# Kernel optimization log

Measured on AMD Instinct MI355X. Metric: run time of the kernel, lower is better.

## Reference

```python
import jax, jax.numpy as jnp
import numpy as np
from functools import partial

HID = 256
HOR = 5

def _lin(k, i, o):
    return jax.random.normal(k, (i, o), jnp.float32) / np.sqrt(i)

def setup_inputs() -> dict:
    key = jax.random.key(0)
    ks = jax.random.split(key, 32)
    B, T, D, Hf, Wf = 4, 16, 768, 16, 16
    H, W = 1024, 1024
    inp = {}
    inp['features'] = jax.random.normal(ks[0], (B, T, D, Hf, Wf), jnp.float32)
    inp['predictions'] = jax.random.uniform(ks[1], (B, T, 1, H, W), dtype=jnp.float32)
    # position encoder: 4 -> HID -> HID
    inp['pe_w1'] = _lin(ks[2], 4, HID); inp['pe_b1'] = jnp.zeros((HID,), jnp.float32)
    inp['pe_w2'] = _lin(ks[3], HID, HID); inp['pe_b2'] = jnp.zeros((HID,), jnp.float32)
    # 2-layer LSTM, gate order i,f,g,o (torch convention)
    inp['wih0'] = _lin(ks[4], HID, 4 * HID); inp['whh0'] = _lin(ks[5], HID, 4 * HID)
    inp['bih0'] = jnp.zeros((4 * HID,), jnp.float32); inp['bhh0'] = jnp.zeros((4 * HID,), jnp.float32)
    inp['wih1'] = _lin(ks[6], HID, 4 * HID); inp['whh1'] = _lin(ks[7], HID, 4 * HID)
    inp['bih1'] = jnp.zeros((4 * HID,), jnp.float32); inp['bhh1'] = jnp.zeros((4 * HID,), jnp.float32)
    # motion predictor: HID -> HID -> HID/2 -> HOR*4
    inp['mp_w1'] = _lin(ks[8], HID, HID); inp['mp_b1'] = jnp.zeros((HID,), jnp.float32)
    inp['mp_w2'] = _lin(ks[9], HID, HID // 2); inp['mp_b2'] = jnp.zeros((HID // 2,), jnp.float32)
    inp['mp_w3'] = _lin(ks[10], HID // 2, HOR * 4); inp['mp_b3'] = jnp.zeros((HOR * 4,), jnp.float32)
    # confidence: HID -> HID/2 -> HOR
    inp['cf_w1'] = _lin(ks[11], HID, HID // 2); inp['cf_b1'] = jnp.zeros((HID // 2,), jnp.float32)
    inp['cf_w2'] = _lin(ks[12], HID // 2, HOR); inp['cf_b2'] = jnp.zeros((HOR,), jnp.float32)
    return inp

def _extract_bboxes(predictions):
    # predictions: (B,T,1,H,W) -> bboxes (B,T,4) in (cx,cy,w,h), normalized
    B, T, _, H, W = predictions.shape
    mask = predictions[:, :, 0] > 0.5  # (B,T,H,W)
    xs = jnp.arange(W, dtype=jnp.float32)           # (W,)
    ys = jnp.arange(H, dtype=jnp.float32)[:, None]  # (H,1)
    big = jnp.float32(H + W)
    x_min = jnp.min(jnp.where(mask, xs, big), axis=(-2, -1))
    x_max = jnp.max(jnp.where(mask, xs, -1.0), axis=(-2, -1))
    y_min = jnp.min(jnp.where(mask, ys, big), axis=(-2, -1))
    y_max = jnp.max(jnp.where(mask, ys, -1.0), axis=(-2, -1))
    has = jnp.any(mask, axis=(-2, -1))  # (B,T)
    cx = (x_min + x_max) / 2.0 / W
    cy = (y_min + y_max) / 2.0 / H
    w = (x_max - x_min) / W
    h = (y_max - y_min) / H
    bbox = jnp.stack([cx, cy, w, h], axis=-1)  # (B,T,4)
    default = jnp.array([0.5, 0.5, 0.1, 0.1], dtype=jnp.float32)
    return jnp.where(has[..., None], bbox, default)

def _lstm_layer(x, wih, whh, bih, bhh):
    # x: (B,T,HID); returns (hs (B,T,H), h_final (B,H))
    B = x.shape[0]
    xg = jnp.einsum('bti,ig->btg', x, wih) + bih  # (B,T,4H)
    def step(carry, xg_t):
        h, c = carry
        g = xg_t + h @ whh + bhh
        i, f, gg, o = jnp.split(g, 4, axis=-1)
        i = jax.nn.sigmoid(i); f = jax.nn.sigmoid(f)
        gg = jnp.tanh(gg); o = jax.nn.sigmoid(o)
        c = f * c + i * gg
        h = o * jnp.tanh(c)
        return (h, c), h
    z = jnp.zeros((B, HID), x.dtype)
    (h, c), hs = jax.lax.scan(step, (z, z), xg.swapaxes(0, 1))
    return hs.swapaxes(0, 1), h

def reference(features, predictions, pe_w1, pe_b1, pe_w2, pe_b2,
              wih0, whh0, bih0, bhh0, wih1, whh1, bih1, bhh1,
              mp_w1, mp_b1, mp_w2, mp_b2, mp_w3, mp_b3,
              cf_w1, cf_b1, cf_w2, cf_b2):
    B, T = features.shape[:2]
    bboxes = _extract_bboxes(predictions)  # (B,T,4)
    pos = jax.nn.relu(bboxes @ pe_w1 + pe_b1)
    pos = jax.nn.relu(pos @ pe_w2 + pe_b2)  # (B,T,HID)
    h1, _ = _lstm_layer(pos, wih0, whh0, bih0, bhh0)
    motion_features, last_hidden = _lstm_layer(h1, wih1, whh1, bih1, bhh1)
    x = jax.nn.relu(last_hidden @ mp_w1 + mp_b1)
    x = jax.nn.relu(x @ mp_w2 + mp_b2)
    predicted_deltas = (x @ mp_w3 + mp_b3).reshape(B, HOR, 4)
    last_bbox = bboxes[:, -1:, :]
    predicted_bboxes = last_bbox + jnp.cumsum(predicted_deltas, axis=1)
    c = jax.nn.relu(last_hidden @ cf_w1 + cf_b1)
    confidence = jax.nn.sigmoid(c @ cf_w2 + cf_b2)  # (B,HOR)
    predicted_locations = predicted_bboxes[..., :2]
    predicted_scales = predicted_bboxes[..., 2:]
    return (predicted_deltas, predicted_bboxes, predicted_locations,
            predicted_scales, motion_features, confidence, bboxes)
```

## Files before the change

### kernel.cpp

```cpp
#include <hip/hip_runtime.h>
#include <math.h>

#define BIGI (1 << 30)

#define PM_OFF    0
#define HT0_OFF   8192
#define HT2_OFF   40960
#define DONE_OFF  45056
#define ZERO_BEG  8192
#define ZERO_END  45057

#define OUT_DELTAS 0
#define OUT_PBB    80
#define OUT_LOC    160
#define OUT_SCL    200
#define OUT_MF     240
#define OUT_CONF   16624
#define OUT_BBOX   16644

__device__ __forceinline__ float sigmoidf_(float x) { return 1.0f / (1.0f + expf(-x)); }

__device__ __forceinline__ void storeh(unsigned long long* p, float h, int tag) {
    unsigned long long v =
        ((unsigned long long)(unsigned)tag << 32) | (unsigned long long)__float_as_uint(h);
    __hip_atomic_store(p, v, __ATOMIC_RELAXED, __HIP_MEMORY_SCOPE_AGENT);
}
__device__ __forceinline__ float pollh(const unsigned long long* p, int tag) {
    unsigned long long v = __hip_atomic_load(p, __ATOMIC_RELAXED, __HIP_MEMORY_SCOPE_AGENT);
    while ((int)(v >> 32) != tag) {
        __builtin_amdgcn_s_sleep(1);
        v = __hip_atomic_load(p, __ATOMIC_RELAXED, __HIP_MEMORY_SCOPE_AGENT);
    }
    return __uint_as_float((unsigned)v);
}
__device__ __forceinline__ float2 pollh2(const unsigned long long* p1, int tag1,
                                         const unsigned long long* p2, int tag2) {
    unsigned long long v1 = __hip_atomic_load(p1, __ATOMIC_RELAXED, __HIP_MEMORY_SCOPE_AGENT);
    unsigned long long v2 = __hip_atomic_load(p2, __ATOMIC_RELAXED, __HIP_MEMORY_SCOPE_AGENT);
    while ((int)(v1 >> 32) != tag1) {
        __builtin_amdgcn_s_sleep(1);
        v1 = __hip_atomic_load(p1, __ATOMIC_RELAXED, __HIP_MEMORY_SCOPE_AGENT);
    }
    while ((int)(v2 >> 32) != tag2) {
        __builtin_amdgcn_s_sleep(1);
        v2 = __hip_atomic_load(p2, __ATOMIC_RELAXED, __HIP_MEMORY_SCOPE_AGENT);
    }
    return make_float2(__uint_as_float((unsigned)v1), __uint_as_float((unsigned)v2));
}

__global__ __launch_bounds__(256) void k_minmax(const float4* __restrict__ pred,
                                                int* __restrict__ ws) {
    int tid = threadIdx.x;
    for (int i = ZERO_BEG + blockIdx.x * 256 + tid; i < ZERO_END; i += 2048 * 256)
        ws[i] = 0;
    int img = blockIdx.x >> 5;
    int chunk = blockIdx.x & 31;
    int base = img * 262144 + chunk * 8192 + tid;
    int xmn = BIGI, xmx = -1, ymn = BIGI, ymx = -1;
#pragma unroll 4
    for (int i = 0; i < 32; ++i) {
        int idx4 = base + i * 256;
        float4 v = pred[idx4];
        int x = (idx4 << 2) & 1023;
        int y = (idx4 >> 8) & 1023;
        bool m0 = v.x > 0.5f, m1 = v.y > 0.5f, m2 = v.z > 0.5f, m3 = v.w > 0.5f;
        int cmn = m0 ? x : (m1 ? x + 1 : (m2 ? x + 2 : (m3 ? x + 3 : BIGI)));
        int cmx = m3 ? x + 3 : (m2 ? x + 2 : (m1 ? x + 1 : (m0 ? x : -1)));
        xmn = min(xmn, cmn);
        xmx = max(xmx, cmx);
        if (m0 | m1 | m2 | m3) { ymn = min(ymn, y); ymx = max(ymx, y); }
    }
    for (int off = 32; off > 0; off >>= 1) {
        xmn = min(xmn, __shfl_down(xmn, off));
        xmx = max(xmx, __shfl_down(xmx, off));
        ymn = min(ymn, __shfl_down(ymn, off));
        ymx = max(ymx, __shfl_down(ymx, off));
    }
    __shared__ int red[4][4];
    int wave = tid >> 6;
    if ((tid & 63) == 0) { red[0][wave] = xmn; red[1][wave] = xmx; red[2][wave] = ymn; red[3][wave] = ymx; }
    __syncthreads();
    if (tid == 0) {
        xmn = min(min(red[0][0], red[0][1]), min(red[0][2], red[0][3]));
        xmx = max(max(red[1][0], red[1][1]), max(red[1][2], red[1][3]));
        ymn = min(min(red[2][0], red[2][1]), min(red[2][2], red[2][3]));
        ymx = max(max(red[3][0], red[3][1]), max(red[3][2], red[3][3]));
        ((int4*)(ws + PM_OFF))[blockIdx.x] = make_int4(xmn, xmx, ymn, ymx);
    }
}

__device__ __forceinline__ void mk_bbox(int xmn, int xmx, int ymn, int ymx, float* o) {
    if (xmx >= 0) {
        o[0] = (float)(xmn + xmx) * (0.5f / 1024.0f);
        o[1] = (float)(ymn + ymx) * (0.5f / 1024.0f);
        o[2] = (float)(xmx - xmn) * (1.0f / 1024.0f);
        o[3] = (float)(ymx - ymn) * (1.0f / 1024.0f);
    } else { o[0] = 0.5f; o[1] = 0.5f; o[2] = 0.1f; o[3] = 0.1f; }
}

__global__ __launch_bounds__(256, 1) void k_fused(
    const float* __restrict__ pe_w1, const float* __restrict__ pe_b1,
    const float* __restrict__ pe_w2, const float* __restrict__ pe_b2,
    const float* __restrict__ wih0, const float* __restrict__ whh0,
    const float* __restrict__ bih0, const float* __restrict__ bhh0,
    const float* __restrict__ wih1, const float* __restrict__ whh1,
    const float* __restrict__ bih1, const float* __restrict__ bhh1,
    const float* __restrict__ mp_w1, const float* __restrict__ mp_b1,
    const float* __restrict__ mp_w2, const float* __restrict__ mp_b2,
    const float* __restrict__ mp_w3, const float* __restrict__ mp_b3,
    const float* __restrict__ cf_w1, const float* __restrict__ cf_b1,
    const float* __restrict__ cf_w2, const float* __restrict__ cf_b2,
    const int4* __restrict__ pm4, unsigned long long* __restrict__ hT0,
    unsigned long long* __restrict__ hT2, int* __restrict__ done,
    float* __restrict__ out) {
    __shared__ __align__(16) float sPX[4096];
    __shared__ __align__(16) float sP1[4096];
    __shared__ float xgl[1024];
    __shared__ __align__(16) float hsm[256];
    __shared__ __align__(16) float h2sm[256];
    __shared__ float partA[256];
    __shared__ float sBB[64];
    const int tid = threadIdx.x, blk = blockIdx.x;

    if (blk >= 128) {
        float a0 = 0.f, a1 = 1.f, a2 = 2.f, a3 = 3.f, a4 = 4.f, a5 = 5.f, a6 = 6.f, a7 = 7.f;
        const float m = 1.0000001f, c = 0.9999999f;
        for (;;) {
#pragma unroll 8
            for (int i = 0; i < 512; ++i) {
                a0 = fmaf(a0, m, c); a1 = fmaf(a1, m, c); a2 = fmaf(a2, m, c); a3 = fmaf(a3, m, c);
                a4 = fmaf(a4, m, c); a5 = fmaf(a5, m, c); a6 = fmaf(a6, m, c); a7 = fmaf(a7, m, c);
            }
            if (__hip_atomic_load(done, __ATOMIC_RELAXED, __HIP_MEMORY_SCOPE_AGENT) >= 4) break;
        }
        asm volatile("" :: "v"(a0), "v"(a1), "v"(a2), "v"(a3), "v"(a4), "v"(a5), "v"(a6), "v"(a7));
        return;
    }

    const int layer = blk >> 6;
    const int b = (blk >> 4) & 3, g = blk & 15;
    const int cidx = tid & 63, kq = tid >> 6;
    const int gate = cidx >> 4, u = cidx & 15;
    const int col = gate * 256 + g * 16 + u;
    const int krow0 = kq * 64;

    const float* wih = layer ? wih1 : wih0;
    const float* whh = layer ? whh1 : whh0;
    const float* bih = layer ? bih1 : bih0;
    const float* bhh = layer ? bhh1 : bhh0;

    float4 wvi[16];
#pragma unroll
    for (int k4 = 0; k4 < 16; ++k4) {
        int r = krow0 + k4 * 4;
        wvi[k4].x = wih[(r + 0) * 1024 + col];
        wvi[k4].y = wih[(r + 1) * 1024 + col];
        wvi[k4].z = wih[(r + 2) * 1024 + col];
        wvi[k4].w = wih[(r + 3) * 1024 + col];
    }

    if (layer == 0) {
        {
            int il = tid >> 4, c2 = (tid & 15) * 2;
            int4 A = pm4[(b * 16 + il) * 32 + c2];
            int4 B = pm4[(b * 16 + il) * 32 + c2 + 1];
            int xmn = min(A.x, B.x), xmx = max(A.y, B.y);
            int ymn = min(A.z, B.z), ymx = max(A.w, B.w);
            for (int off = 8; off > 0; off >>= 1) {
                xmn = min(xmn, __shfl_down(xmn, off, 16));
                xmx = max(xmx, __shfl_down(xmx, off, 16));
                ymn = min(ymn, __shfl_down(ymn, off, 16));
                ymx = max(ymx, __shfl_down(ymx, off, 16));
            }
            if ((tid & 15) == 0) {
                float bb[4];
                mk_bbox(xmn, xmx, ymn, ymx, bb);
                sBB[il * 4 + 0] = bb[0]; sBB[il * 4 + 1] = bb[1];
                sBB[il * 4 + 2] = bb[2]; sBB[il * 4 + 3] = bb[3];
                if (g == 0) {
                    out[OUT_BBOX + (b * 16 + il) * 4 + 0] = bb[0];
                    out[OUT_BBOX + (b * 16 + il) * 4 + 1] = bb[1];
                    out[OUT_BBOX + (b * 16 + il) * 4 + 2] = bb[2];
                    out[OUT_BBOX + (b * 16 + il) * 4 + 3] = bb[3];
                }
            }
        }
        __syncthreads();
        {
            float w0 = pe_w1[tid], w1 = pe_w1[256 + tid];
            float w2 = pe_w1[512 + tid], w3 = pe_w1[768 + tid], b1v = pe_b1[tid];
#pragma unroll
            for (int i = 0; i < 16; ++i) {
                float v = sBB[i * 4] * w0 + sBB[i * 4 + 1] * w1 +
                          sBB[i * 4 + 2] * w2 + sBB[i * 4 + 3] * w3 + b1v;
                sP1[i * 256 + tid] = fmaxf(v, 0.0f);
            }
        }
        __syncthreads();
        {
            float acc[16];
            float b2v = pe_b2[tid];
#pragma unroll
            for (int i = 0; i < 16; ++i) acc[i] = b2v;
            for (int k = 0; k < 256; ++k) {
                float wv = pe_w2[k * 256 + tid];
#pragma unroll
                for (int i = 0; i < 16; ++i) acc[i] += sP1[i * 256 + k] * wv;
            }
#pragma unroll
            for (int i = 0; i < 16; ++i) sPX[i * 256 + tid] = fmaxf(acc[i], 0.0f);
        }
        __syncthreads();
        float bsum = 0.0f;
        if (tid < 64) {
            int cc = (tid >> 4) * 256 + g * 16 + (tid & 15);
            bsum = bih[cc] + bhh[cc];
        }
        for (int t = 0; t < 16; ++t) {
            const float4* xr = (const float4*)&sPX[t * 256 + krow0];
            float a = 0.0f;
#pragma unroll
            for (int k = 0; k < 16; ++k) {
                float4 x = xr[k];
                a += x.x * wvi[k].x + x.y * wvi[k].y + x.z * wvi[k].z + x.w * wvi[k].w;
            }
            partA[tid] = a;
            __syncthreads();
            if (tid < 64)
                xgl[t * 64 + tid] = partA[tid] + partA[64 + tid] +
                                    partA[128 + tid] + partA[192 + tid] + bsum;
            __syncthreads();
        }
    }

    float4 wvh[16];
#pragma unroll
    for (int k4 = 0; k4 < 16; ++k4) {
        int r = krow0 + k4 * 4;
        wvh[k4].x = whh[(r + 0) * 1024 + col];
        wvh[k4].y = whh[(r + 1) * 1024 + col];
        wvh[k4].z = whh[(r + 2) * 1024 + col];
        wvh[k4].w = whh[(r + 3) * 1024 + col];
    }
    float bs0 = 0.f, bs1 = 0.f, bs2 = 0.f, bs3 = 0.f;
    if (layer == 1 && tid < 16) {
        int uu = g * 16 + tid;
        bs0 = bih[uu] + bhh[uu];
        bs1 = bih[256 + uu] + bhh[256 + uu];
        bs2 = bih[512 + uu] + bhh[512 + uu];
        bs3 = bih[768 + uu] + bhh[768 + uu];
    }

    float cst = 0.0f;
    for (int t = 0; t < 16; ++t) {
        if (layer == 0) {
            if (t) hsm[tid] = pollh(&hT0[((b * 16 + t - 1) << 8) + tid], t);
        } else {
            if (t) {
                float2 hv = pollh2(&hT0[((b * 16 + t) << 8) + tid], t + 1,
                                   &hT2[(((b << 1) | ((t - 1) & 1)) << 8) + tid], t);
                hsm[tid] = hv.x; h2sm[tid] = hv.y;
            } else {
                hsm[tid] = pollh(&hT0[((b * 16) << 8) + tid], 1);
            }
        }
        __syncthreads();
        float a = 0.0f;
        if (layer == 0) {
            if (t) {
                const float4* hr = (const float4*)&hsm[krow0];
#pragma unroll
                for (int k = 0; k < 16; ++k) {
                    float4 h = hr[k];
                    a += h.x * wvh[k].x + h.y * wvh[k].y + h.z * wvh[k].z + h.w * wvh[k].w;
                }
            }
        } else {
            const float4* xr = (const float4*)&hsm[krow0];
#pragma unroll
            for (int k = 0; k < 16; ++k) {
                float4 x = xr[k];
                a += x.x * wvi[k].x + x.y * wvi[k].y + x.z * wvi[k].z + x.w * wvi[k].w;
            }
            if (t) {
                const float4* hr = (const float4*)&h2sm[krow0];
#pragma unroll
                for (int k = 0; k < 16; ++k) {
                    float4 h = hr[k];
                    a += h.x * wvh[k].x + h.y * wvh[k].y + h.z * wvh[k].z + h.w * wvh[k].w;
                }
            }
        }
        partA[tid] = a;
        __syncthreads();
        if (tid < 16) {
            float gi, gf, gg, go;
            if (layer == 0) {
                gi = xgl[t * 64 + tid];       gf = xgl[t * 64 + 16 + tid];
                gg = xgl[t * 64 + 32 + tid];  go = xgl[t * 64 + 48 + tid];
            } else { gi = bs0; gf = bs1; gg = bs2; go = bs3; }
#pragma unroll
            for (int q = 0; q < 4; ++q) {
                gi += partA[q * 64 + tid];
                gf += partA[q * 64 + 16 + tid];
                gg += partA[q * 64 + 32 + tid];
                go += partA[q * 64 + 48 + tid];
            }
            float i_ = sigmoidf_(gi), f_ = sigmoidf_(gf);
            float g_ = tanhf(gg), o_ = sigmoidf_(go);
            cst = f_ * cst + i_ * g_;
            float h = o_ * tanhf(cst);
            int unit = g * 16 + tid;
            if (layer == 0) {
                storeh(&hT0[((b * 16 + t) << 8) + unit], h, t + 1);
            } else {
                storeh(&hT2[(((b << 1) | (t & 1)) << 8) + unit], h, t + 1);
                out[OUT_MF + (b * 16 + t) * 256 + unit] = h;
            }
        }
    }
    if (layer == 0 || g != 0) return;

    float* lh = sPX;
    float* x1 = sPX + 256;
    float* c1 = sPX + 512;
    float* x2 = sPX + 640;
    float* dl = sPX + 768;
    lh[tid] = pollh(&hT2[(((b << 1) | 1) << 8) + tid], 16);
    if (tid < 32) {
        int4 v = pm4[(b * 16 + 15) * 32 + tid];
        int xmn = v.x, xmx = v.y, ymn = v.z, ymx = v.w;
        for (int off = 16; off > 0; off >>= 1) {
            xmn = min(xmn, __shfl_down(xmn, off, 32));
            xmx = max(xmx, __shfl_down(xmx, off, 32));
            ymn = min(ymn, __shfl_down(ymn, off, 32));
            ymx = max(ymx, __shfl_down(ymx, off, 32));
        }
        if (tid == 0) mk_bbox(xmn, xmx, ymn, ymx, sBB);
    }
    __syncthreads();
    {
        float a = mp_b1[tid];
#pragma unroll 4
        for (int k = 0; k < 256; ++k) a += lh[k] * mp_w1[k * 256 + tid];
        x1[tid] = fmaxf(a, 0.0f);
    }
    if (tid < 128) {
        float a = cf_b1[tid];
#pragma unroll 4
        for (int k = 0; k < 256; ++k) a += lh[k] * cf_w1[k * 128 + tid];
        c1[tid] = fmaxf(a, 0.0f);
    }
    __syncthreads();
    if (tid < 128) {
        float a = mp_b2[tid];
#pragma unroll 4
        for (int k = 0; k < 256; ++k) a += x1[k] * mp_w2[k * 128 + tid];
        x2[tid] = fmaxf(a, 0.0f);
    } else if (tid < 133) {
        int jj = tid - 128;
        float a = cf_b2[jj];
#pragma unroll 4
        for (int k = 0; k < 128; ++k) a += c1[k] * cf_w2[k * 5 + jj];
        out[OUT_CONF + b * 5 + jj] = sigmoidf_(a);
    }
    __syncthreads();
    if (tid < 20) {
        float a = mp_b3[tid];
#pragma unroll 4
        for (int k = 0; k < 128; ++k) a += x2[k] * mp_w3[k * 20 + tid];
        dl[tid] = a;
        out[OUT_DELTAS + b * 20 + tid] = a;
    }
    __syncthreads();
    if (tid < 4) {
        float acc = sBB[tid];
        for (int hh = 0; hh < 5; ++hh) {
            acc += dl[hh * 4 + tid];
            out[OUT_PBB + b * 20 + hh * 4 + tid] = acc;
            if (tid < 2) out[OUT_LOC + b * 10 + hh * 2 + tid] = acc;
            else out[OUT_SCL + b * 10 + hh * 2 + (tid - 2)] = acc;
        }
    }
    __syncthreads();
    if (tid == 0) atomicAdd(done, 1);
}

extern "C" void kernel_launch(void* const* d_in, const int* in_sizes, int n_in,
                              void* d_out, int out_size, void* d_ws, size_t ws_size,
                              hipStream_t stream) {
    (void)in_sizes; (void)n_in; (void)out_size; (void)ws_size;
    const float* pred = (const float*)d_in[1];
    const float* pe_w1 = (const float*)d_in[2];
    const float* pe_b1 = (const float*)d_in[3];
    const float* pe_w2 = (const float*)d_in[4];
    const float* pe_b2 = (const float*)d_in[5];
    const float* wih0 = (const float*)d_in[6];
    const float* whh0 = (const float*)d_in[7];
    const float* bih0 = (const float*)d_in[8];
    const float* bhh0 = (const float*)d_in[9];
    const float* wih1 = (const float*)d_in[10];
    const float* whh1 = (const float*)d_in[11];
    const float* bih1 = (const float*)d_in[12];
    const float* bhh1 = (const float*)d_in[13];
    const float* mp_w1 = (const float*)d_in[14];
    const float* mp_b1 = (const float*)d_in[15];
    const float* mp_w2 = (const float*)d_in[16];
    const float* mp_b2 = (const float*)d_in[17];
    const float* mp_w3 = (const float*)d_in[18];
    const float* mp_b3 = (const float*)d_in[19];
    const float* cf_w1 = (const float*)d_in[20];
    const float* cf_b1 = (const float*)d_in[21];
    const float* cf_w2 = (const float*)d_in[22];
    const float* cf_b2 = (const float*)d_in[23];
    float* out = (float*)d_out;
    int* wsi = (int*)d_ws;

    hipLaunchKernelGGL(k_minmax, dim3(64 * 32), dim3(256), 0, stream,
                       (const float4*)pred, wsi);
    hipLaunchKernelGGL(k_fused, dim3(256), dim3(256), 0, stream,
                       pe_w1, pe_b1, pe_w2, pe_b2,
                       wih0, whh0, bih0, bhh0,
                       wih1, whh1, bih1, bhh1,
                       mp_w1, mp_b1, mp_w2, mp_b2, mp_w3, mp_b3,
                       cf_w1, cf_b1, cf_w2, cf_b2,
                       (const int4*)(wsi + PM_OFF),
                       (unsigned long long*)(wsi + HT0_OFF),
                       (unsigned long long*)(wsi + HT2_OFF),
                       wsi + DONE_OFF, out);
}
```

Baseline: 594.4 us.

## Drop spinner blocks and batch layer-0 input projection before recurrence

Removes the 128 busy-spin 'heater' blocks and the done counter, so the fused kernel launches only the 128 LSTM worker blocks. Layer-0 now computes the input projection for all 16 timesteps as one batched pass into shared memory, then loads the recurrent weights only afterwards, so the two weight sets are never held in registers together. The confidence head's first layer moves onto otherwise idle threads. The spinners were presumably meant to keep clocks high or hold CUs, so removing them risks lower clocks or slower inter-block polling latency.

```diff
diff --git a/kernel.cpp b/kernel.cpp
--- a/kernel.cpp
+++ b/kernel.cpp
@@ -6,9 +6,8 @@
 #define PM_OFF    0
 #define HT0_OFF   8192
 #define HT2_OFF   40960
-#define DONE_OFF  45056
 #define ZERO_BEG  8192
-#define ZERO_END  45057
+#define ZERO_END  45056
 
 #define OUT_DELTAS 0
 #define OUT_PBB    80
@@ -51,8 +50,10 @@
 __global__ __launch_bounds__(256) void k_minmax(const float4* __restrict__ pred,
                                                 int* __restrict__ ws) {
     int tid = threadIdx.x;
-    for (int i = ZERO_BEG + blockIdx.x * 256 + tid; i < ZERO_END; i += 2048 * 256)
-        ws[i] = 0;
+    {
+        int i = ZERO_BEG + blockIdx.x * 256 + tid;
+        if (i < ZERO_END) ws[i] = 0;
+    }
     int img = blockIdx.x >> 5;
     int chunk = blockIdx.x & 31;
     int base = img * 262144 + chunk * 8192 + tid;
@@ -111,55 +112,24 @@
     const float* __restrict__ cf_w1, const float* __restrict__ cf_b1,
     const float* __restrict__ cf_w2, const float* __restrict__ cf_b2,
     const int4* __restrict__ pm4, unsigned long long* __restrict__ hT0,
-    unsigned long long* __restrict__ hT2, int* __restrict__ done,
-    float* __restrict__ out) {
-    __shared__ __align__(16) float sPX[4096];
-    __shared__ __align__(16) float sP1[4096];
+    unsigned long long* __restrict__ hT2, float* __restrict__ out) {
+    __shared__ __align__(16) float sA[4096];
+    __shared__ __align__(16) float sB[4096];
     __shared__ float xgl[1024];
     __shared__ __align__(16) float hsm[256];
     __shared__ __align__(16) float h2sm[256];
-    __shared__ float partA[256];
+    __shared__ float part[256];
     __shared__ float sBB[64];
     const int tid = threadIdx.x, blk = blockIdx.x;
-
-    if (blk >= 128) {
-        float a0 = 0.f, a1 = 1.f, a2 = 2.f, a3 = 3.f, a4 = 4.f, a5 = 5.f, a6 = 6.f, a7 = 7.f;
-        const float m = 1.0000001f, c = 0.9999999f;
-        for (;;) {
-#pragma unroll 8
-            for (int i = 0; i < 512; ++i) {
-                a0 = fmaf(a0, m, c); a1 = fmaf(a1, m, c); a2 = fmaf(a2, m, c); a3 = fmaf(a3, m, c);
-                a4 = fmaf(a4, m, c); a5 = fmaf(a5, m, c); a6 = fmaf(a6, m, c); a7 = fmaf(a7, m, c);
-            }
-            if (__hip_atomic_load(done, __ATOMIC_RELAXED, __HIP_MEMORY_SCOPE_AGENT) >= 4) break;
-        }
-        asm volatile("" :: "v"(a0), "v"(a1), "v"(a2), "v"(a3), "v"(a4), "v"(a5), "v"(a6), "v"(a7));
-        return;
-    }
-
-    const int layer = blk >> 6;
+    const int stage = blk >> 6;
     const int b = (blk >> 4) & 3, g = blk & 15;
-    const int cidx = tid & 63, kq = tid >> 6;
-    const int gate = cidx >> 4, u = cidx & 15;
-    const int col = gate * 256 + g * 16 + u;
+    const int cq = tid & 63, kq = tid >> 6;
+    const int col = ((cq >> 4) << 8) + g * 16 + (cq & 15);
     const int krow0 = kq * 64;
 
-    const float* wih = layer ? wih1 : wih0;
-    const float* whh = layer ? whh1 : whh0;
-    const float* bih = layer ? bih1 : bih0;
-    const float* bhh = layer ? bhh1 : bhh0;
-
-    float4 wvi[16];
-#pragma unroll
-    for (int k4 = 0; k4 < 16; ++k4) {
-        int r = krow0 + k4 * 4;
-        wvi[k4].x = wih[(r + 0) * 1024 + col];
-        wvi[k4].y = wih[(r + 1) * 1024 + col];
-        wvi[k4].z = wih[(r + 2) * 1024 + col];
-        wvi[k4].w = wih[(r + 3) * 1024 + col];
-    }
-
-    if (layer == 0) {
+    float cst = 0.0f;
+
+    if (stage == 0) {
         {
             int il = tid >> 4, c2 = (tid & 15) * 2;
             int4 A = pm4[(b * 16 + il) * 32 + c2];
@@ -193,7 +163,7 @@
             for (int i = 0; i < 16; ++i) {
                 float v = sBB[i * 4] * w0 + sBB[i * 4 + 1] * w1 +
                           sBB[i * 4 + 2] * w2 + sBB[i * 4 + 3] * w3 + b1v;
-                sP1[i * 256 + tid] = fmaxf(v, 0.0f);
+                sB[i * 256 + tid] = fmaxf(v, 0.0f);
             }
         }
         __syncthreads();
@@ -205,127 +175,159 @@
             for (int k = 0; k < 256; ++k) {
                 float wv = pe_w2[k * 256 + tid];
 #pragma unroll
-                for (int i = 0; i < 16; ++i) acc[i] += sP1[i * 256 + k] * wv;
-            }
-#pragma unroll
-            for (int i = 0; i < 16; ++i) sPX[i * 256 + tid] = fmaxf(acc[i], 0.0f);
-        }
-        __syncthreads();
-        float bsum = 0.0f;
-        if (tid < 64) {
-            int cc = (tid >> 4) * 256 + g * 16 + (tid & 15);
-            bsum = bih[cc] + bhh[cc];
-        }
+                for (int i = 0; i < 16; ++i) acc[i] += sB[i * 256 + k] * wv;
+            }
+#pragma unroll
+            for (int i = 0; i < 16; ++i) sA[i * 256 + tid] = fmaxf(acc[i], 0.0f);
+        }
+        __syncthreads();
+        {
+            float4 wt[16];
+#pragma unroll
+            for (int k4 = 0; k4 < 16; ++k4) {
+                int r = krow0 + k4 * 4;
+                wt[k4].x = wih0[(r + 0) * 1024 + col];
+                wt[k4].y = wih0[(r + 1) * 1024 + col];
+                wt[k4].z = wih0[(r + 2) * 1024 + col];
+                wt[k4].w = wih0[(r + 3) * 1024 + col];
+            }
+            float xacc[16];
+#pragma unroll
+            for (int t = 0; t < 16; ++t) {
+                const float4* pr = (const float4*)&sA[t * 256 + krow0];
+                float a = 0.0f;
+#pragma unroll
+                for (int k = 0; k < 16; ++k) {
+                    float4 x = pr[k];
+                    a += x.x * wt[k].x + x.y * wt[k].y + x.z * wt[k].z + x.w * wt[k].w;
+                }
+                xacc[t] = a;
+            }
+#pragma unroll
+            for (int t = 0; t < 16; ++t) sB[t * 256 + tid] = xacc[t];
+        }
+        __syncthreads();
+        {
+            int cq2 = tid & 63, tq = tid >> 6;
+            int col2 = ((cq2 >> 4) << 8) + g * 16 + (cq2 & 15);
+            float bsum = bih0[col2] + bhh0[col2];
+#pragma unroll
+            for (int j = 0; j < 4; ++j) {
+                int t = tq + 4 * j;
+                xgl[t * 64 + cq2] = sB[t * 256 + cq2] + sB[t * 256 + 64 + cq2] +
+                                    sB[t * 256 + 128 + cq2] + sB[t * 256 + 192 + cq2] + bsum;
+            }
+        }
+        float4 wh[16];
+#pragma unroll
+        for (int k4 = 0; k4 < 16; ++k4) {
+            int r = krow0 + k4 * 4;
+            wh[k4].x = whh0[(r + 0) * 1024 + col];
+            wh[k4].y = whh0[(r + 1) * 1024 + col];
+            wh[k4].z = whh0[(r + 2) * 1024 + col];
+            wh[k4].w = whh0[(r + 3) * 1024 + col];
+        }
+        __syncthreads();
         for (int t = 0; t < 16; ++t) {
-            const float4* xr = (const float4*)&sPX[t * 256 + krow0];
+            if (t) hsm[tid] = pollh(&hT0[((b * 16 + t - 1) << 8) + tid], t);
+            __syncthreads();
             float a = 0.0f;
+            if (t) {
+                const float4* hr = (const float4*)&hsm[krow0];
+#pragma unroll
+                for (int k = 0; k < 16; ++k) {
+                    float4 h = hr[k];
+                    a += h.x * wh[k].x + h.y * wh[k].y + h.z * wh[k].z + h.w * wh[k].w;
+                }
+            }
+            part[tid] = a;
+            __syncthreads();
+            if (tid < 16) {
+                int u = tid;
+                float gi = xgl[t * 64 + u]      + part[u]      + part[64 + u]  + part[128 + u] + part[192 + u];
+                float gf = xgl[t * 64 + 16 + u] + part[16 + u] + part[80 + u]  + part[144 + u] + part[208 + u];
+                float gg = xgl[t * 64 + 32 + u] + part[32 + u] + part[96 + u]  + part[160 + u] + part[224 + u];
+                float go = xgl[t * 64 + 48 + u] + part[48 + u] + part[112 + u] + part[176 + u] + part[240 + u];
+                float i_ = sigmoidf_(gi), f_ = sigmoidf_(gf);
+                float g_ = tanhf(gg), o_ = sigmoidf_(go);
+                cst = f_ * cst + i_ * g_;
+                float h = o_ * tanhf(cst);
+                storeh(&hT0[((b * 16 + t) << 8) + g * 16 + u], h, t + 1);
+            }
+        }
+        return;
+    }
+
+    float4 wi[16], wh[16];
+#pragma unroll
+    for (int k4 = 0; k4 < 16; ++k4) {
+        int r = krow0 + k4 * 4;
+        wi[k4].x = wih1[(r + 0) * 1024 + col];
+        wi[k4].y = wih1[(r + 1) * 1024 + col];
+        wi[k4].z = wih1[(r + 2) * 1024 + col];
+        wi[k4].w = wih1[(r + 3) * 1024 + col];
+        wh[k4].x = whh1[(r + 0) * 1024 + col];
+        wh[k4].y = whh1[(r + 1) * 1024 + col];
+        wh[k4].z = whh1[(r + 2) * 1024 + col];
+        wh[k4].w = whh1[(r + 3) * 1024 + col];
+    }
+    float bs0 = 0.f, bs1 = 0.f, bs2 = 0.f, bs3 = 0.f;
+    if (tid < 16) {
+        int uu = g * 16 + tid;
+        bs0 = bih1[uu] + bhh1[uu];
+        bs1 = bih1[256 + uu] + bhh1[256 + uu];
+        bs2 = bih1[512 + uu] + bhh1[512 + uu];
+        bs3 = bih1[768 + uu] + bhh1[768 + uu];
+    }
+    for (int t = 0; t < 16; ++t) {
+        if (t) {
+            float2 hv = pollh2(&hT0[((b * 16 + t) << 8) + tid], t + 1,
+                               &hT2[(((b << 1) | ((t - 1) & 1)) << 8) + tid], t);
+            hsm[tid] = hv.x; h2sm[tid] = hv.y;
+        } else {
+            hsm[tid] = pollh(&hT0[((b * 16) << 8) + tid], 1);
+        }
+        __syncthreads();
+        float a = 0.0f;
+        {
+            const float4* xr = (const float4*)&hsm[krow0];
 #pragma unroll
             for (int k = 0; k < 16; ++k) {
                 float4 x = xr[k];
-                a += x.x * wvi[k].x + x.y * wvi[k].y + x.z * wvi[k].z + x.w * wvi[k].w;
-            }
-            partA[tid] = a;
-            __syncthreads();
-            if (tid < 64)
-                xgl[t * 64 + tid] = partA[tid] + partA[64 + tid] +
-                                    partA[128 + tid] + partA[192 + tid] + bsum;
-            __syncthreads();
-        }
-    }
-
-    float4 wvh[16];
-#pragma unroll
-    for (int k4 = 0; k4 < 16; ++k4) {
-        int r = krow0 + k4 * 4;
-        wvh[k4].x = whh[(r + 0) * 1024 + col];
-        wvh[k4].y = whh[(r + 1) * 1024 + col];
-        wvh[k4].z = whh[(r + 2) * 1024 + col];
-        wvh[k4].w = whh[(r + 3) * 1024 + col];
-    }
-    float bs0 = 0.f, bs1 = 0.f, bs2 = 0.f, bs3 = 0.f;
-    if (layer == 1 && tid < 16) {
-        int uu = g * 16 + tid;
-        bs0 = bih[uu] + bhh[uu];
-        bs1 = bih[256 + uu] + bhh[256 + uu];
-        bs2 = bih[512 + uu] + bhh[512 + uu];
-        bs3 = bih[768 + uu] + bhh[768 + uu];
-    }
-
-    float cst = 0.0f;
-    for (int t = 0; t < 16; ++t) {
-        if (layer == 0) {
-            if (t) hsm[tid] = pollh(&hT0[((b * 16 + t - 1) << 8) + tid], t);
-        } else {
-            if (t) {
-                float2 hv = pollh2(&hT0[((b * 16 + t) << 8) + tid], t + 1,
-                                   &hT2[(((b << 1) | ((t - 1) & 1)) << 8) + tid], t);
-                hsm[tid] = hv.x; h2sm[tid] = hv.y;
-            } else {
-                hsm[tid] = pollh(&hT0[((b * 16) << 8) + tid], 1);
-            }
-        }
-        __syncthreads();
-        float a = 0.0f;
-        if (layer == 0) {
-            if (t) {
-                const float4* hr = (const float4*)&hsm[krow0];
-#pragma unroll
-                for (int k = 0; k < 16; ++k) {
-                    float4 h = hr[k];
-                    a += h.x * wvh[k].x + h.y * wvh[k].y + h.z * wvh[k].z + h.w * wvh[k].w;
-                }
-            }
-        } else {
-            const float4* xr = (const float4*)&hsm[krow0];
+                a += x.x * wi[k].x + x.y * wi[k].y + x.z * wi[k].z + x.w * wi[k].w;
+            }
+        }
+        if (t) {
+            const float4* hr = (const float4*)&h2sm[krow0];
 #pragma unroll
             for (int k = 0; k < 16; ++k) {
-                float4 x = xr[k];
-                a += x.x * wvi[k].x + x.y * wvi[k].y + x.z * wvi[k].z + x.w * wvi[k].w;
-            }
-            if (t) {
-                const float4* hr = (const float4*)&h2sm[krow0];
-#pragma unroll
-                for (int k = 0; k < 16; ++k) {
-                    float4 h = hr[k];
-                    a += h.x * wvh[k].x + h.y * wvh[k].y + h.z * wvh[k].z + h.w * wvh[k].w;
-                }
-            }
-        }
-        partA[tid] = a;
+                float4 h = hr[k];
+                a += h.x * wh[k].x + h.y * wh[k].y + h.z * wh[k].z + h.w * wh[k].w;
+            }
+        }
+        part[tid] = a;
         __syncthreads();
         if (tid < 16) {
-            float gi, gf, gg, go;
-            if (layer == 0) {
-                gi = xgl[t * 64 + tid];       gf = xgl[t * 64 + 16 + tid];
-                gg = xgl[t * 64 + 32 + tid];  go = xgl[t * 64 + 48 + tid];
-            } else { gi = bs0; gf = bs1; gg = bs2; go = bs3; }
-#pragma unroll
-            for (int q = 0; q < 4; ++q) {
-                gi += partA[q * 64 + tid];
-                gf += partA[q * 64 + 16 + tid];
-                gg += partA[q * 64 + 32 + tid];
-                go += partA[q * 64 + 48 + tid];
-            }
+            int u = tid, unit = g * 16 + u;
+            float gi = bs0 + part[u]      + part[64 + u]  + part[128 + u] + part[192 + u];
+            float gf = bs1 + part[16 + u] + part[80 + u]  + part[144 + u] + part[208 + u];
+            float gg = bs2 + part[32 + u] + part[96 + u]  + part[160 + u] + part[224 + u];
+            float go = bs3 + part[48 + u] + part[112 + u] + part[176 + u] + part[240 + u];
             float i_ = sigmoidf_(gi), f_ = sigmoidf_(gf);
             float g_ = tanhf(gg), o_ = sigmoidf_(go);
             cst = f_ * cst + i_ * g_;
             float h = o_ * tanhf(cst);
-            int unit = g * 16 + tid;
-            if (layer == 0) {
-                storeh(&hT0[((b * 16 + t) << 8) + unit], h, t + 1);
-            } else {
-                storeh(&hT2[(((b << 1) | (t & 1)) << 8) + unit], h, t + 1);
-                out[OUT_MF + (b * 16 + t) * 256 + unit] = h;
-            }
-        }
-    }
-    if (layer == 0 || g != 0) return;
-
-    float* lh = sPX;
-    float* x1 = sPX + 256;
-    float* c1 = sPX + 512;
-    float* x2 = sPX + 640;
-    float* dl = sPX + 768;
+            storeh(&hT2[(((b << 1) | (t & 1)) << 8) + unit], h, t + 1);
+            out[OUT_MF + (b * 16 + t) * 256 + unit] = h;
+        }
+    }
+    if (g != 0) return;
+
+    float* lh = sA;
+    float* x1 = sA + 256;
+    float* c1 = sA + 512;
+    float* x2 = sA + 640;
+    float* dl = sA + 768;
     lh[tid] = pollh(&hT2[(((b << 1) | 1) << 8) + tid], 16);
     if (tid < 32) {
         int4 v = pm4[(b * 16 + 15) * 32 + tid];
@@ -345,24 +347,18 @@
         for (int k = 0; k < 256; ++k) a += lh[k] * mp_w1[k * 256 + tid];
         x1[tid] = fmaxf(a, 0.0f);
     }
-    if (tid < 128) {
-        float a = cf_b1[tid];
-#pragma unroll 4
-        for (int k = 0; k < 256; ++k) a += lh[k] * cf_w1[k * 128 + tid];
-        c1[tid] = fmaxf(a, 0.0f);
-    }
     __syncthreads();
     if (tid < 128) {
         float a = mp_b2[tid];
 #pragma unroll 4
         for (int k = 0; k < 256; ++k) a += x1[k] * mp_w2[k * 128 + tid];
         x2[tid] = fmaxf(a, 0.0f);
-    } else if (tid < 133) {
+    } else {
         int jj = tid - 128;
-        float a = cf_b2[jj];
-#pragma unroll 4
-        for (int k = 0; k < 128; ++k) a += c1[k] * cf_w2[k * 5 + jj];
-        out[OUT_CONF + b * 5 + jj] = sigmoidf_(a);
+        float a = cf_b1[jj];
+#pragma unroll 4
+        for (int k = 0; k < 256; ++k) a += lh[k] * cf_w1[k * 128 + jj];
+        c1[jj] = fmaxf(a, 0.0f);
     }
     __syncthreads();
     if (tid < 20) {
@@ -371,6 +367,15 @@
         for (int k = 0; k < 128; ++k) a += x2[k] * mp_w3[k * 20 + tid];
         dl[tid] = a;
         out[OUT_DELTAS + b * 20 + tid] = a;
+    } else if (tid >= 32 && tid < 52) {
+        int idx = tid - 32, bb2 = idx / 5, j = idx - bb2 * 5;
+        (void)bb2;
+        if (idx < 5) {
+            float a = cf_b2[idx];
+#pragma unroll 4
+            for (int k = 0; k < 128; ++k) a += c1[k] * cf_w2[k * 5 + idx];
+            out[OUT_CONF + b * 5 + idx] = sigmoidf_(a);
+        }
     }
     __syncthreads();
     if (tid < 4) {
@@ -382,8 +387,6 @@
             else out[OUT_SCL + b * 10 + hh * 2 + (tid - 2)] = acc;
         }
     }
-    __syncthreads();
-    if (tid == 0) atomicAdd(done, 1);
 }
 
 extern "C" void kernel_launch(void* const* d_in, const int* in_sizes, int n_in,
@@ -418,7 +421,7 @@
 
     hipLaunchKernelGGL(k_minmax, dim3(64 * 32), dim3(256), 0, stream,
                        (const float4*)pred, wsi);
-    hipLaunchKernelGGL(k_fused, dim3(256), dim3(256), 0, stream,
+    hipLaunchKernelGGL(k_fused, dim3(128), dim3(256), 0, stream,
                        pe_w1, pe_b1, pe_w2, pe_b2,
                        wih0, whh0, bih0, bhh0,
                        wih1, whh1, bih1, bhh1,
@@ -427,5 +430,5 @@
                        (const int4*)(wsi + PM_OFF),
                        (unsigned long long*)(wsi + HT0_OFF),
                        (unsigned long long*)(wsi + HT2_OFF),
-                       wsi + DONE_OFF, out);
-}
+                       out);
+}
```

Result: faster. 561.2 us (-5.6%).
